# Kernel optimization log

Hardware: AMD Instinct MI355X
Metric: run time of the kernel (lower is better)

## Reference

```python
import jax, jax.numpy as jnp
import numpy as np

RES = 16            # voxel grid resolution (init arg res)
G = RES ** 3        # number of cells = 4096
REG_R = float(np.sqrt(3.0)) / RES  # sqrt(3)/s regularizer radius
B, C, RND, NPTS, H = 16, 64, 2, 16384, 256


def _grid_offsets():
    # util.meshgrid(res): integer grid coords, then ((grid+0.5)/res - 0.5).view(3,-1)
    r = jnp.arange(RES)
    gx, gy, gz = jnp.meshgrid(r, r, r, indexing='ij')
    grid = jnp.stack([gx, gy, gz], 0).reshape(3, -1).astype(jnp.float32)  # [3, G]
    return (grid + 0.5) / RES - 0.5


def _dens_sample(dens, n_points):
    # Deterministic largest-remainder allocation of n_points proportional to density.
    b = dens.shape[0]
    p = dens.reshape(b, -1)
    p = p / jnp.sum(p, axis=-1, keepdims=True)
    scaled = p * n_points                      # [b, G]
    base = jnp.floor(scaled)
    rem = (n_points - jnp.sum(base, axis=-1)).astype(jnp.int32)   # [b]
    frac = scaled - base
    ranks = jnp.argsort(jnp.argsort(-frac, axis=-1), axis=-1)      # rank by fractional part
    return base.astype(jnp.int32) + (ranks < rem[:, None]).astype(jnp.int32)  # [b, G]


def setup_inputs() -> dict:
    key = jax.random.key(0)
    ks = jax.random.split(key, 9)
    cin = C + RND
    f32 = jnp.float32
    return {
        'x': jax.random.normal(ks[0], (B, C, RES, RES, RES), f32),
        'dens': jax.random.uniform(ks[1], (B, RES, RES, RES), f32) + 1e-3,
        'noise': jax.random.uniform(ks[2], (B, RND, NPTS), f32),
        'W1': jax.random.normal(ks[3], (H, cin), f32) * np.float32(1.0 / np.sqrt(cin)),
        'b1': jnp.zeros((H,), f32),
        'W2': jax.random.normal(ks[4], (H, H), f32) * np.float32(1.0 / np.sqrt(H)),
        'b2': jnp.zeros((H,), f32),
        'W3': jax.random.normal(ks[5], (3, H), f32) * np.float32(1.0 / np.sqrt(H)),
        'b3': jnp.zeros((3,), f32),
        'n_points': NPTS,
    }


def reference(x, dens, noise, W1, b1, W2, b2, W3, b3, n_points):
    b, c = x.shape[0], x.shape[1]
    x_flat = x.reshape(b, c, -1)                        # [b, c, G]
    n = _dens_sample(dens, n_points)                    # [b, G] repeat counts, sums to n_points
    # Vectorized replacement for the nonzero()/cat loop: cell i appears n[i] times.
    cell_ids = jnp.arange(G)
    idx = jax.vmap(lambda ni: jnp.repeat(cell_ids, ni, total_repeat_length=n_points))(n)  # [b, n_points]
    x_ind = jnp.take_along_axis(x_flat, idx[:, None, :], axis=2)   # [b, c, n_points]
    o = _grid_offsets()                                 # [3, G]
    gen_off = jnp.transpose(o[:, idx], (1, 0, 2))       # [b, 3, n_points]
    rnd = noise * 2.0 - 1.0                             # uniform in [-1, 1)
    gen_inp = jnp.concatenate([x_ind, rnd], axis=1)     # [b, c+rnd, n_points]
    # pointwise conv1d MLP generator
    h = jax.nn.relu(jnp.einsum('oc,bcn->bon', W1, gen_inp) + b1[:, None])
    h = jax.nn.relu(jnp.einsum('oh,bhn->bon', W2, h) + b2[:, None])
    out = jnp.einsum('oh,bhn->bon', W3, h) + b3[:, None]            # [b, 3, n_points]
    norm = jnp.sqrt(jnp.sum(out * out, axis=1))                      # [b, n_points]
    reg = jnp.maximum(norm - REG_R, 0.0)
    return (out + gen_off, reg)
```

## Files before the change

### kernel.cpp

```cpp
#include <hip/hip_runtime.h>

typedef unsigned long long u64;
typedef _Float16 f16x8 __attribute__((ext_vector_type(8)));
typedef float    f32x4 __attribute__((ext_vector_type(4)));

#define G_    4096
#define NPTS  16384

union H8 { _Float16 h[8]; uint4 u; };
union H4 { _Float16 h[4]; uint2 u; };


__global__ __launch_bounds__(256) void kP(const float* __restrict__ dens,
                                          int* __restrict__ pc,
                                          const float* __restrict__ W1,
                                          const float* __restrict__ W2,
                                          const float* __restrict__ W3,
                                          _Float16* __restrict__ w1f,
                                          _Float16* __restrict__ w2f,
                                          _Float16* __restrict__ w3f,
                                          float* __restrict__ w1n){
  __shared__ double sred[256];
  __shared__ u64  keys[4096];
  __shared__ int  nvs[4096];
  __shared__ int  binidx[4096];
  __shared__ int  hist[1024];
  __shared__ int  cab[1024];
  __shared__ int  scan[256];
  __shared__ float Sf;
  __shared__ int  remS, BstarS, needS, cntS;
  const int t = threadIdx.x;

  if (blockIdx.x >= 16){
    const int e = (blockIdx.x - 16)*256 + t;
    H8 v;
    if (e < 8192){
      const int RT = e >> 9, kt = (e >> 6) & 7, l = e & 63;
      const int m = RT*16 + (l & 15), k = kt*32 + ((l >> 4) << 3);
      #pragma unroll
      for (int j = 0; j < 8; ++j) v.h[j] = (_Float16)W2[m*256 + k + j];
      *(uint4*)&w2f[e*8] = v.u;
    } else if (e < 10240){
      const int e2 = e - 8192;
      const int RT = e2 >> 7, r2 = e2 & 127, kt = r2 >> 6, l = r2 & 63;
      const int m = RT*16 + (l & 15), k = kt*32 + ((l >> 4) << 3);
      #pragma unroll
      for (int j = 0; j < 8; ++j) v.h[j] = (_Float16)W1[m*66 + k + j];
      *(uint4*)&w1f[e2*8] = v.u;
    } else if (e < 10752){
      const int e3 = e - 10240;
      const int kt = e3 >> 6, l = e3 & 63;
      const int m = l & 15, k = kt*32 + ((l >> 4) << 3);
      #pragma unroll
      for (int j = 0; j < 8; ++j) v.h[j] = (m < 3) ? (_Float16)W3[m*256 + k + j] : (_Float16)0.f;
      *(uint4*)&w3f[e3*8] = v.u;
    } else if (e < 11008){
      const int r = e - 10752;
      w1n[r*2 + 0] = W1[r*66 + 64];
      w1n[r*2 + 1] = W1[r*66 + 65];
    }
    return;
  }

  const int b = blockIdx.x;
  const float* d = dens + b*G_;

  for (int j = t; j < 1024; j += 256) hist[j] = 0;
  if (t == 0) cntS = 0;

  double s = 0.0;
  for (int j = 0; j < 16; ++j) s += (double)d[t + 256*j];
  sred[t] = s; __syncthreads();
  for (int off = 128; off > 0; off >>= 1){
    if (t < off) sred[t] += sred[t + off];
    __syncthreads();
  }
  if (t == 0) Sf = (float)sred[0];
  __syncthreads();
  const float S = Sf;

  int bi[16]; int bs = 0;
  #pragma unroll
  for (int j = 0; j < 16; ++j){
    const int i = t + 256*j;
    const float p  = d[i] / S;
    const float sc = p * 16384.0f;
    const float fl = floorf(sc);
    const float fr = sc - fl;
    bi[j] = (int)fl; bs += bi[j];
    const unsigned fb = __float_as_uint(fr);
    keys[i] = ((u64)fb << 12) | (u64)(4095 - i);
    atomicAdd(&hist[fb >> 20], 1);
  }
  scan[t] = bs; __syncthreads();
  for (int off = 128; off > 0; off >>= 1){
    if (t < off) scan[t] += scan[t + off];
    __syncthreads();
  }
  if (t == 0) remS = 16384 - scan[0];
  __syncthreads();
  const int rem = remS;

  const int h0 = hist[4*t], h1 = hist[4*t+1], h2 = hist[4*t+2], h3 = hist[4*t+3];
  const int gs = h0 + h1 + h2 + h3;
  __syncthreads();
  scan[t] = gs; __syncthreads();
  for (int off = 1; off < 256; off <<= 1){
    const int v2 = (t + off < 256) ? scan[t + off] : 0;
    __syncthreads();
    scan[t] += v2;
    __syncthreads();
  }
  const int sAfter = scan[t] - gs;
  cab[4*t+3] = sAfter;
  cab[4*t+2] = sAfter + h3;
  cab[4*t+1] = sAfter + h3 + h2;
  cab[4*t+0] = sAfter + h3 + h2 + h1;
  if (t == 0){ BstarS = 0x7fffffff; needS = 0; }
  __syncthreads();
  if (rem > 0){
    const int ca[4] = {cab[4*t], cab[4*t+1], cab[4*t+2], cab[4*t+3]};
    const int hh[4] = {h0, h1, h2, h3};
    #pragma unroll
    for (int q = 0; q < 4; ++q)
      if (ca[q] < rem && rem <= ca[q] + hh[q]){ BstarS = 4*t + q; needS = rem - ca[q]; }
  }
  __syncthreads();
  const int Bstar = BstarS, need = needS;

  #pragma unroll
  for (int j = 0; j < 16; ++j){
    const int i = t + 256*j;
    const int bin = (int)(keys[i] >> 32);
    nvs[i] = bi[j] + ((bin > Bstar) ? 1 : 0);
    if (bin == Bstar){ const int pos = atomicAdd(&cntS, 1); binidx[pos] = i; }
  }
  __syncthreads();
  const int cnt = cntS;
  for (int p = t; p < cnt; p += 256){
    const u64 K = keys[binidx[p]];
    int r = 0;
    for (int q = 0; q < cnt; ++q) r += (keys[binidx[q]] > K) ? 1 : 0;
    if (r < need) nvs[binidx[p]] += 1;
  }
  __syncthreads();

  int loc[16]; int ls = 0;
  #pragma unroll
  for (int j = 0; j < 16; ++j){ loc[j] = nvs[t*16 + j]; ls += loc[j]; }
  __syncthreads();
  scan[t] = ls; __syncthreads();
  for (int off = 1; off < 256; off <<= 1){
    const int v2 = (t >= off) ? scan[t - off] : 0;
    __syncthreads();
    scan[t] += v2;
    __syncthreads();
  }
  int off0 = scan[t] - ls;
  int* o = pc + b*NPTS;
  #pragma unroll
  for (int j = 0; j < 16; ++j){
    const int c = t*16 + j;
    for (int r = 0; r < loc[j]; ++r) o[off0++] = c;
  }
}

__global__ __launch_bounds__(256, 3) void kE(
    const float* __restrict__ x, const float* __restrict__ noise,
    const _Float16* __restrict__ w1f, const _Float16* __restrict__ w2f,
    const _Float16* __restrict__ w3f, const float* __restrict__ w1n,
    const float* __restrict__ b1, const float* __restrict__ b2, const float* __restrict__ b3,
    const int* __restrict__ pc, float* __restrict__ out)
{
  __shared__ _Float16 Hb[16384];
  __shared__ int   cells[64];
  __shared__ float rndS[2][64];
  const int b = blockIdx.y, p0 = blockIdx.x*64, tid = threadIdx.x;
  const int w = tid >> 6, lane = tid & 63;

  if (tid < 64) cells[tid] = pc[b*NPTS + p0 + tid];
  if (tid >= 64 && tid < 192){
    const int rr = (tid - 64) >> 6, p = tid & 63;
    rndS[rr][p] = noise[(b*2 + rr)*NPTS + p0 + p]*2.f - 1.f;
  }
  __syncthreads();

  {
    const int koct = tid & 3, pt = tid >> 2;
    const int ct = pt >> 4, lane2 = (pt & 15) + koct*16;
    const int cell = cells[pt];
    #pragma unroll
    for (int kt = 0; kt < 2; ++kt){
      const int kbase = kt*32 + koct*8;
      const float* xb = x + ((size_t)(b*64 + kbase))*G_ + cell;
      H8 v;
      #pragma unroll
      for (int j = 0; j < 8; ++j) v.h[j] = (_Float16)xb[(size_t)j*G_];
      *(uint4*)&Hb[((kt*4 + ct)*64 + lane2)*8] = v.u;
    }
  }
  __syncthreads();

  f32x4 acc[4][4];
  const f32x4 zz = {0.f, 0.f, 0.f, 0.f};
  #pragma unroll
  for (int rt = 0; rt < 4; ++rt)
    #pragma unroll
    for (int ct = 0; ct < 4; ++ct) acc[rt][ct] = zz;

  const int wr = w*4;

  __builtin_amdgcn_s_setprio(1);
  #pragma unroll
  for (int kt = 0; kt < 2; ++kt){
    f16x8 B[4];
    #pragma unroll
    for (int ct = 0; ct < 4; ++ct) B[ct] = *(f16x8*)&Hb[((kt*4 + ct)*64 + lane)*8];
    #pragma unroll
    for (int rt = 0; rt < 4; ++rt){
      f16x8 A = *(const f16x8*)&w1f[(((wr + rt)*2 + kt)*64 + lane)*8];
      #pragma unroll
      for (int ct = 0; ct < 4; ++ct)
        acc[rt][ct] = __builtin_amdgcn_mfma_f32_16x16x32_f16(A, B[ct], acc[rt][ct], 0, 0, 0);
    }
  }
  __builtin_amdgcn_s_setprio(0);

  {
    const int m16 = lane & 15, khi = lane >> 4;
    float rn0[4], rn1[4];
    #pragma unroll
    for (int ct = 0; ct < 4; ++ct){
      rn0[ct] = rndS[0][ct*16 + m16];
      rn1[ct] = rndS[1][ct*16 + m16];
    }
    #pragma unroll
    for (int rt = 0; rt < 4; ++rt){
      const int row0 = w*64 + rt*16 + khi*4;
      const float4 wa = *(const float4*)&w1n[row0*2];
      const float4 wb = *(const float4*)&w1n[row0*2 + 4];
      #pragma unroll
      for (int ct = 0; ct < 4; ++ct){
        acc[rt][ct][0] += wa.x*rn0[ct] + wa.y*rn1[ct];
        acc[rt][ct][1] += wa.z*rn0[ct] + wa.w*rn1[ct];
        acc[rt][ct][2] += wb.x*rn0[ct] + wb.y*rn1[ct];
        acc[rt][ct][3] += wb.z*rn0[ct] + wb.w*rn1[ct];
      }
    }
  }
  __syncthreads();

  #pragma unroll
  for (int rt = 0; rt < 4; ++rt){
    const int row0 = w*64 + rt*16 + ((lane >> 4) << 2);
    const float4 bq = *(const float4*)&b1[row0];
    const int kt2 = row0 >> 5, c16 = (row0 >> 3) & 3, j0 = row0 & 7;
    const int lane2 = (lane & 15) + c16*16;
    #pragma unroll
    for (int ct = 0; ct < 4; ++ct){
      H4 v;
      v.h[0] = (_Float16)fmaxf(acc[rt][ct][0] + bq.x, 0.f);
      v.h[1] = (_Float16)fmaxf(acc[rt][ct][1] + bq.y, 0.f);
      v.h[2] = (_Float16)fmaxf(acc[rt][ct][2] + bq.z, 0.f);
      v.h[3] = (_Float16)fmaxf(acc[rt][ct][3] + bq.w, 0.f);
      *(uint2*)&Hb[((kt2*4 + ct)*64 + lane2)*8 + j0] = v.u;
      acc[rt][ct] = zz;
    }
  }
  __syncthreads();

  __builtin_amdgcn_s_setprio(1);
  #pragma unroll 4
  for (int kt = 0; kt < 8; ++kt){
    f16x8 B[4];
    #pragma unroll
    for (int ct = 0; ct < 4; ++ct) B[ct] = *(f16x8*)&Hb[((kt*4 + ct)*64 + lane)*8];
    #pragma unroll
    for (int rt = 0; rt < 4; ++rt){
      f16x8 A = *(const f16x8*)&w2f[(((wr + rt)*8 + kt)*64 + lane)*8];
      #pragma unroll
      for (int ct = 0; ct < 4; ++ct)
        acc[rt][ct] = __builtin_amdgcn_mfma_f32_16x16x32_f16(A, B[ct], acc[rt][ct], 0, 0, 0);
    }
  }
  __builtin_amdgcn_s_setprio(0);
  __syncthreads();

  #pragma unroll
  for (int rt = 0; rt < 4; ++rt){
    const int row0 = w*64 + rt*16 + ((lane >> 4) << 2);
    const float4 bq = *(const float4*)&b2[row0];
    const int kt2 = row0 >> 5, c16 = (row0 >> 3) & 3, j0 = row0 & 7;
    const int lane2 = (lane & 15) + c16*16;
    #pragma unroll
    for (int ct = 0; ct < 4; ++ct){
      H4 v;
      v.h[0] = (_Float16)fmaxf(acc[rt][ct][0] + bq.x, 0.f);
      v.h[1] = (_Float16)fmaxf(acc[rt][ct][1] + bq.y, 0.f);
      v.h[2] = (_Float16)fmaxf(acc[rt][ct][2] + bq.z, 0.f);
      v.h[3] = (_Float16)fmaxf(acc[rt][ct][3] + bq.w, 0.f);
      *(uint2*)&Hb[((kt2*4 + ct)*64 + lane2)*8 + j0] = v.u;
    }
  }
  __syncthreads();

  f32x4 a3 = zz;
  __builtin_amdgcn_s_setprio(1);
  #pragma unroll
  for (int kt = 0; kt < 8; ++kt){
    f16x8 B = *(f16x8*)&Hb[((kt*4 + w)*64 + lane)*8];
    f16x8 A = *(const f16x8*)&w3f[(kt*64 + lane)*8];
    a3 = __builtin_amdgcn_mfma_f32_16x16x32_f16(A, B, a3, 0, 0, 0);
  }
  __builtin_amdgcn_s_setprio(0);
  if (lane < 16){
    const float ox = a3[0] + b3[0];
    const float oy = a3[1] + b3[1];
    const float oz = a3[2] + b3[2];
    const float nrm = sqrtf(ox*ox + oy*oy + oz*oz);
    const float rg_ = fmaxf(nrm - (float)0.10825317547305482, 0.f);
    const int pt = w*16 + lane;
    const int cell = cells[pt];
    const float fx = ((float)(cell >> 8)        + 0.5f) * 0.0625f - 0.5f;
    const float fy = ((float)((cell >> 4) & 15) + 0.5f) * 0.0625f - 0.5f;
    const float fz = ((float)(cell & 15)        + 0.5f) * 0.0625f - 0.5f;
    const int pidx = p0 + pt;
    out[b*49152 +          pidx] = ox + fx;
    out[b*49152 + 16384 +  pidx] = oy + fy;
    out[b*49152 + 32768 +  pidx] = oz + fz;
    out[786432  + b*16384 + pidx] = rg_;
  }
}

extern "C" void kernel_launch(void* const* d_in, const int* in_sizes, int n_in,
                              void* d_out, int out_size, void* d_ws, size_t ws_size,
                              hipStream_t stream){
  const float* x     = (const float*)d_in[0];
  const float* dens  = (const float*)d_in[1];
  const float* noise = (const float*)d_in[2];
  const float* W1    = (const float*)d_in[3];
  const float* b1    = (const float*)d_in[4];
  const float* W2    = (const float*)d_in[5];
  const float* b2    = (const float*)d_in[6];
  const float* W3    = (const float*)d_in[7];
  const float* b3    = (const float*)d_in[8];

  char* ws = (char*)d_ws;
  int*      pc   = (int*)(ws + 0);
  _Float16* w1f  = (_Float16*)(ws + 1048576);
  _Float16* w2f  = (_Float16*)(ws + 1081344);
  _Float16* w3f  = (_Float16*)(ws + 1212416);
  float*    w1n  = (float*)(ws + 1220608);
  float*    out  = (float*)d_out;

  kP<<<dim3(59),      dim3(256), 0, stream>>>(dens, pc, W1, W2, W3, w1f, w2f, w3f, w1n);
  kE<<<dim3(256, 16), dim3(256), 0, stream>>>(x, noise, w1f, w2f, w3f, w1n,
                                              b1, b2, b3, pc, out);
}
```

Baseline: 86.26 us.

## Software-pipeline W2 fragment loads, prefetch W3, drop sync and use packed f16 converts

The layer-2 MFMA loop is fully unrolled with double-buffered A-fragment registers, so the W2 loads for step k+2 are issued between MFMAs of step k. The first two W2 fragments are loaded early, before the noise/bias epilogue of layer 1, and all W3 fragments are loaded into registers before the layer-2 epilogue. The first __syncthreads is removed: each thread reads its cell index straight from global memory rather than through shared memory. Scalar f16 casts become packed round-toward-zero converts, which changes rounding slightly and raises register pressure under the 3-block occupancy bound.

```diff
diff --git a/kernel.cpp b/kernel.cpp
--- a/kernel.cpp
+++ b/kernel.cpp
@@ -3,12 +3,16 @@
 typedef unsigned long long u64;
 typedef _Float16 f16x8 __attribute__((ext_vector_type(8)));
 typedef float    f32x4 __attribute__((ext_vector_type(4)));
+typedef __fp16   fp16x2 __attribute__((ext_vector_type(2)));
 
 #define G_    4096
 #define NPTS  16384
 
 union H8 { _Float16 h[8]; uint4 u; };
-union H4 { _Float16 h[4]; uint2 u; };
+union PK2 { fp16x2 h[2]; uint2 u; };
+union PK4 { fp16x2 h[4]; uint4 u; };
+
+#define MFMA_(A_,B_,C_) __builtin_amdgcn_mfma_f32_16x16x32_f16((A_),(B_),(C_),0,0,0)
 
 
 __global__ __launch_bounds__(256) void kP(const float* __restrict__ dens,
@@ -178,24 +182,28 @@
   const int b = blockIdx.y, p0 = blockIdx.x*64, tid = threadIdx.x;
   const int w = tid >> 6, lane = tid & 63;
 
+  const int pt_g  = tid >> 2;
+  const int cell_g = pc[b*NPTS + p0 + pt_g];
   if (tid < 64) cells[tid] = pc[b*NPTS + p0 + tid];
   if (tid >= 64 && tid < 192){
     const int rr = (tid - 64) >> 6, p = tid & 63;
     rndS[rr][p] = noise[(b*2 + rr)*NPTS + p0 + p]*2.f - 1.f;
   }
-  __syncthreads();
-
   {
-    const int koct = tid & 3, pt = tid >> 2;
-    const int ct = pt >> 4, lane2 = (pt & 15) + koct*16;
-    const int cell = cells[pt];
+    const int koct = tid & 3;
+    const int ct = pt_g >> 4, lane2 = (pt_g & 15) + koct*16;
     #pragma unroll
     for (int kt = 0; kt < 2; ++kt){
       const int kbase = kt*32 + koct*8;
-      const float* xb = x + ((size_t)(b*64 + kbase))*G_ + cell;
-      H8 v;
-      #pragma unroll
-      for (int j = 0; j < 8; ++j) v.h[j] = (_Float16)xb[(size_t)j*G_];
+      const float* xb = x + ((size_t)(b*64 + kbase))*G_ + cell_g;
+      float xv[8];
+      #pragma unroll
+      for (int j = 0; j < 8; ++j) xv[j] = xb[(size_t)j*G_];
+      PK4 v;
+      v.h[0] = __builtin_amdgcn_cvt_pkrtz(xv[0], xv[1]);
+      v.h[1] = __builtin_amdgcn_cvt_pkrtz(xv[2], xv[3]);
+      v.h[2] = __builtin_amdgcn_cvt_pkrtz(xv[4], xv[5]);
+      v.h[3] = __builtin_amdgcn_cvt_pkrtz(xv[6], xv[7]);
       *(uint4*)&Hb[((kt*4 + ct)*64 + lane2)*8] = v.u;
     }
   }
@@ -221,10 +229,17 @@
       f16x8 A = *(const f16x8*)&w1f[(((wr + rt)*2 + kt)*64 + lane)*8];
       #pragma unroll
       for (int ct = 0; ct < 4; ++ct)
-        acc[rt][ct] = __builtin_amdgcn_mfma_f32_16x16x32_f16(A, B[ct], acc[rt][ct], 0, 0, 0);
+        acc[rt][ct] = MFMA_(A, B[ct], acc[rt][ct]);
     }
   }
   __builtin_amdgcn_s_setprio(0);
+
+  f16x8 A0[4], A1[4];
+  #pragma unroll
+  for (int rt = 0; rt < 4; ++rt){
+    A0[rt] = *(const f16x8*)&w2f[(((wr + rt)*8 + 0)*64 + lane)*8];
+    A1[rt] = *(const f16x8*)&w2f[(((wr + rt)*8 + 1)*64 + lane)*8];
+  }
 
   {
     const int m16 = lane & 15, khi = lane >> 4;
@@ -258,11 +273,11 @@
     const int lane2 = (lane & 15) + c16*16;
     #pragma unroll
     for (int ct = 0; ct < 4; ++ct){
-      H4 v;
-      v.h[0] = (_Float16)fmaxf(acc[rt][ct][0] + bq.x, 0.f);
-      v.h[1] = (_Float16)fmaxf(acc[rt][ct][1] + bq.y, 0.f);
-      v.h[2] = (_Float16)fmaxf(acc[rt][ct][2] + bq.z, 0.f);
-      v.h[3] = (_Float16)fmaxf(acc[rt][ct][3] + bq.w, 0.f);
+      PK2 v;
+      v.h[0] = __builtin_amdgcn_cvt_pkrtz(fmaxf(acc[rt][ct][0] + bq.x, 0.f),
+                                          fmaxf(acc[rt][ct][1] + bq.y, 0.f));
+      v.h[1] = __builtin_amdgcn_cvt_pkrtz(fmaxf(acc[rt][ct][2] + bq.z, 0.f),
+                                          fmaxf(acc[rt][ct][3] + bq.w, 0.f));
       *(uint2*)&Hb[((kt2*4 + ct)*64 + lane2)*8 + j0] = v.u;
       acc[rt][ct] = zz;
     }
@@ -270,20 +285,40 @@
   __syncthreads();
 
   __builtin_amdgcn_s_setprio(1);
-  #pragma unroll 4
-  for (int kt = 0; kt < 8; ++kt){
-    f16x8 B[4];
-    #pragma unroll
-    for (int ct = 0; ct < 4; ++ct) B[ct] = *(f16x8*)&Hb[((kt*4 + ct)*64 + lane)*8];
-    #pragma unroll
-    for (int rt = 0; rt < 4; ++rt){
-      f16x8 A = *(const f16x8*)&w2f[(((wr + rt)*8 + kt)*64 + lane)*8];
-      #pragma unroll
-      for (int ct = 0; ct < 4; ++ct)
-        acc[rt][ct] = __builtin_amdgcn_mfma_f32_16x16x32_f16(A, B[ct], acc[rt][ct], 0, 0, 0);
-    }
-  }
+#define MFMA4(AR, RT) \
+    acc[RT][0] = MFMA_(AR, Bv0, acc[RT][0]); \
+    acc[RT][1] = MFMA_(AR, Bv1, acc[RT][1]); \
+    acc[RT][2] = MFMA_(AR, Bv2, acc[RT][2]); \
+    acc[RT][3] = MFMA_(AR, Bv3, acc[RT][3]);
+#define L2STEP(KT, ACUR) { \
+    f16x8 Bv0 = *(f16x8*)&Hb[(((KT)*4 + 0)*64 + lane)*8]; \
+    f16x8 Bv1 = *(f16x8*)&Hb[(((KT)*4 + 1)*64 + lane)*8]; \
+    f16x8 Bv2 = *(f16x8*)&Hb[(((KT)*4 + 2)*64 + lane)*8]; \
+    f16x8 Bv3 = *(f16x8*)&Hb[(((KT)*4 + 3)*64 + lane)*8]; \
+    MFMA4(ACUR[0], 0); \
+    if ((KT) + 2 < 8) ACUR[0] = *(const f16x8*)&w2f[(((wr + 0)*8 + (KT) + 2)*64 + lane)*8]; \
+    MFMA4(ACUR[1], 1); \
+    if ((KT) + 2 < 8) ACUR[1] = *(const f16x8*)&w2f[(((wr + 1)*8 + (KT) + 2)*64 + lane)*8]; \
+    MFMA4(ACUR[2], 2); \
+    if ((KT) + 2 < 8) ACUR[2] = *(const f16x8*)&w2f[(((wr + 2)*8 + (KT) + 2)*64 + lane)*8]; \
+    MFMA4(ACUR[3], 3); \
+    if ((KT) + 2 < 8) ACUR[3] = *(const f16x8*)&w2f[(((wr + 3)*8 + (KT) + 2)*64 + lane)*8]; \
+  }
+  L2STEP(0, A0)
+  L2STEP(1, A1)
+  L2STEP(2, A0)
+  L2STEP(3, A1)
+  L2STEP(4, A0)
+  L2STEP(5, A1)
+  L2STEP(6, A0)
+  L2STEP(7, A1)
+#undef L2STEP
+#undef MFMA4
   __builtin_amdgcn_s_setprio(0);
+
+  f16x8 W3v[8];
+  #pragma unroll
+  for (int kt = 0; kt < 8; ++kt) W3v[kt] = *(const f16x8*)&w3f[(kt*64 + lane)*8];
   __syncthreads();
 
   #pragma unroll
@@ -294,11 +329,11 @@
     const int lane2 = (lane & 15) + c16*16;
     #pragma unroll
     for (int ct = 0; ct < 4; ++ct){
-      H4 v;
-      v.h[0] = (_Float16)fmaxf(acc[rt][ct][0] + bq.x, 0.f);
-      v.h[1] = (_Float16)fmaxf(acc[rt][ct][1] + bq.y, 0.f);
-      v.h[2] = (_Float16)fmaxf(acc[rt][ct][2] + bq.z, 0.f);
-      v.h[3] = (_Float16)fmaxf(acc[rt][ct][3] + bq.w, 0.f);
+      PK2 v;
+      v.h[0] = __builtin_amdgcn_cvt_pkrtz(fmaxf(acc[rt][ct][0] + bq.x, 0.f),
+                                          fmaxf(acc[rt][ct][1] + bq.y, 0.f));
+      v.h[1] = __builtin_amdgcn_cvt_pkrtz(fmaxf(acc[rt][ct][2] + bq.z, 0.f),
+                                          fmaxf(acc[rt][ct][3] + bq.w, 0.f));
       *(uint2*)&Hb[((kt2*4 + ct)*64 + lane2)*8 + j0] = v.u;
     }
   }
@@ -309,8 +344,7 @@
   #pragma unroll
   for (int kt = 0; kt < 8; ++kt){
     f16x8 B = *(f16x8*)&Hb[((kt*4 + w)*64 + lane)*8];
-    f16x8 A = *(const f16x8*)&w3f[(kt*64 + lane)*8];
-    a3 = __builtin_amdgcn_mfma_f32_16x16x32_f16(A, B, a3, 0, 0, 0);
+    a3 = MFMA_(W3v[kt], B, a3);
   }
   __builtin_amdgcn_s_setprio(0);
   if (lane < 16){
```

Result: slower. 90.47 us (+4.9%).

## Pre-transpose x to cell-major fp16 and fold noise into padded W1 MFMA

Applied to the files above, without the earlier changes.

Adds extra prep blocks that transpose x into a per-cell contiguous fp16 layout, so the main kernel gathers 16-byte vectors per point instead of 8 strided fp32 loads. The two noise channels are packed into a third zero-padded K tile of W1, which replaces the scalar fp32 noise FMAs with one more MFMA step. It also preloads the W3 fragments into registers before the last barrier and uses packed round-toward-zero fp16 conversions. The cost is an extra 8 MB workspace write and read in the prep kernel, plus a third MFMA K step that is mostly zeros.

```diff
diff --git a/kernel.cpp b/kernel.cpp
--- a/kernel.cpp
+++ b/kernel.cpp
@@ -3,23 +3,34 @@
 typedef unsigned long long u64;
 typedef _Float16 f16x8 __attribute__((ext_vector_type(8)));
 typedef float    f32x4 __attribute__((ext_vector_type(4)));
+typedef __fp16   fp16x2 __attribute__((ext_vector_type(2)));
 
 #define G_    4096
 #define NPTS  16384
 
 union H8 { _Float16 h[8]; uint4 u; };
-union H4 { _Float16 h[4]; uint2 u; };
-
+union PK2 { fp16x2 h[2]; uint2 u; };
+union PK4 { fp16x2 h[4]; uint4 u; };
+
+#define MFMA_(A_,B_,C_) __builtin_amdgcn_mfma_f32_16x16x32_f16((A_),(B_),(C_),0,0,0)
+
+
+#define OFF_W1F 1048576
+#define OFF_W2F 1097728
+#define OFF_W3F 1228800
+#define OFF_XT  1236992
+#define WS_NEED (OFF_XT + 8388608)
 
 __global__ __launch_bounds__(256) void kP(const float* __restrict__ dens,
                                           int* __restrict__ pc,
                                           const float* __restrict__ W1,
                                           const float* __restrict__ W2,
                                           const float* __restrict__ W3,
+                                          const float* __restrict__ x,
                                           _Float16* __restrict__ w1f,
                                           _Float16* __restrict__ w2f,
                                           _Float16* __restrict__ w3f,
-                                          float* __restrict__ w1n){
+                                          _Float16* __restrict__ xT){
   __shared__ double sred[256];
   __shared__ u64  keys[4096];
   __shared__ int  nvs[4096];
@@ -31,6 +42,27 @@
   __shared__ int  remS, BstarS, needS, cntS;
   const int t = threadIdx.x;
 
+  if (blockIdx.x >= 62){
+    const int idx = blockIdx.x - 62;
+    const int b = idx >> 4, blk = idx & 15;
+    const int cell = blk*256 + t;
+    const float* xb = x + ((size_t)b*64)*G_ + cell;
+    _Float16* xo = xT + ((size_t)(b*G_ + cell))*64;
+    #pragma unroll
+    for (int c8 = 0; c8 < 8; ++c8){
+      float a[8];
+      #pragma unroll
+      for (int j = 0; j < 8; ++j) a[j] = xb[(size_t)(c8*8 + j)*G_];
+      PK4 v;
+      v.h[0] = __builtin_amdgcn_cvt_pkrtz(a[0], a[1]);
+      v.h[1] = __builtin_amdgcn_cvt_pkrtz(a[2], a[3]);
+      v.h[2] = __builtin_amdgcn_cvt_pkrtz(a[4], a[5]);
+      v.h[3] = __builtin_amdgcn_cvt_pkrtz(a[6], a[7]);
+      *(uint4*)&xo[c8*8] = v.u;
+    }
+    return;
+  }
+
   if (blockIdx.x >= 16){
     const int e = (blockIdx.x - 16)*256 + t;
     H8 v;
@@ -40,24 +72,20 @@
       #pragma unroll
       for (int j = 0; j < 8; ++j) v.h[j] = (_Float16)W2[m*256 + k + j];
       *(uint4*)&w2f[e*8] = v.u;
-    } else if (e < 10240){
+    } else if (e < 11264){
       const int e2 = e - 8192;
-      const int RT = e2 >> 7, r2 = e2 & 127, kt = r2 >> 6, l = r2 & 63;
+      const int RT = e2 / 192, r2 = e2 % 192, kt = r2 >> 6, l = r2 & 63;
       const int m = RT*16 + (l & 15), k = kt*32 + ((l >> 4) << 3);
       #pragma unroll
-      for (int j = 0; j < 8; ++j) v.h[j] = (_Float16)W1[m*66 + k + j];
+      for (int j = 0; j < 8; ++j) v.h[j] = (k + j < 66) ? (_Float16)W1[m*66 + k + j] : (_Float16)0.f;
       *(uint4*)&w1f[e2*8] = v.u;
-    } else if (e < 10752){
-      const int e3 = e - 10240;
+    } else if (e < 11776){
+      const int e3 = e - 11264;
       const int kt = e3 >> 6, l = e3 & 63;
       const int m = l & 15, k = kt*32 + ((l >> 4) << 3);
       #pragma unroll
       for (int j = 0; j < 8; ++j) v.h[j] = (m < 3) ? (_Float16)W3[m*256 + k + j] : (_Float16)0.f;
       *(uint4*)&w3f[e3*8] = v.u;
-    } else if (e < 11008){
-      const int r = e - 10752;
-      w1n[r*2 + 0] = W1[r*66 + 64];
-      w1n[r*2 + 1] = W1[r*66 + 65];
     }
     return;
   }
@@ -165,37 +193,54 @@
   }
 }
 
+template<bool USE_XT>
 __global__ __launch_bounds__(256, 3) void kE(
-    const float* __restrict__ x, const float* __restrict__ noise,
+    const float* __restrict__ x, const _Float16* __restrict__ xT,
+    const float* __restrict__ noise,
     const _Float16* __restrict__ w1f, const _Float16* __restrict__ w2f,
-    const _Float16* __restrict__ w3f, const float* __restrict__ w1n,
+    const _Float16* __restrict__ w3f,
     const float* __restrict__ b1, const float* __restrict__ b2, const float* __restrict__ b3,
     const int* __restrict__ pc, float* __restrict__ out)
 {
   __shared__ _Float16 Hb[16384];
-  __shared__ int   cells[64];
-  __shared__ float rndS[2][64];
+  __shared__ int cells[64];
   const int b = blockIdx.y, p0 = blockIdx.x*64, tid = threadIdx.x;
   const int w = tid >> 6, lane = tid & 63;
 
   if (tid < 64) cells[tid] = pc[b*NPTS + p0 + tid];
-  if (tid >= 64 && tid < 192){
-    const int rr = (tid - 64) >> 6, p = tid & 63;
-    rndS[rr][p] = noise[(b*2 + rr)*NPTS + p0 + p]*2.f - 1.f;
-  }
-  __syncthreads();
 
   {
-    const int koct = tid & 3, pt = tid >> 2;
-    const int ct = pt >> 4, lane2 = (pt & 15) + koct*16;
-    const int cell = cells[pt];
-    #pragma unroll
-    for (int kt = 0; kt < 2; ++kt){
-      const int kbase = kt*32 + koct*8;
-      const float* xb = x + ((size_t)(b*64 + kbase))*G_ + cell;
-      H8 v;
-      #pragma unroll
-      for (int j = 0; j < 8; ++j) v.h[j] = (_Float16)xb[(size_t)j*G_];
+    const int ct = tid >> 6, l2 = tid & 63;
+    const int k2 = l2 >> 4, pt = ct*16 + (l2 & 15);
+    PK4 v; v.u = make_uint4(0u, 0u, 0u, 0u);
+    if (k2 == 0){
+      const float n0 = noise[(b*2 + 0)*NPTS + p0 + pt]*2.f - 1.f;
+      const float n1 = noise[(b*2 + 1)*NPTS + p0 + pt]*2.f - 1.f;
+      v.h[0] = __builtin_amdgcn_cvt_pkrtz(n0, n1);
+    }
+    *(uint4*)&Hb[((2*4 + ct)*64 + l2)*8] = v.u;
+  }
+
+  #pragma unroll
+  for (int i = 0; i < 2; ++i){
+    const int e = tid + 256*i;
+    const int pt = e >> 3, koct = e & 7;
+    const int cell = pc[b*NPTS + p0 + pt];
+    const int kt = koct >> 2, k2 = koct & 3;
+    const int lane2 = (pt & 15) + k2*16, ct = pt >> 4;
+    if (USE_XT){
+      const uint4 v = *(const uint4*)&xT[((size_t)(b*G_ + cell))*64 + koct*8];
+      *(uint4*)&Hb[((kt*4 + ct)*64 + lane2)*8] = v;
+    } else {
+      const float* xb = x + ((size_t)(b*64 + koct*8))*G_ + cell;
+      float a[8];
+      #pragma unroll
+      for (int j = 0; j < 8; ++j) a[j] = xb[(size_t)j*G_];
+      PK4 v;
+      v.h[0] = __builtin_amdgcn_cvt_pkrtz(a[0], a[1]);
+      v.h[1] = __builtin_amdgcn_cvt_pkrtz(a[2], a[3]);
+      v.h[2] = __builtin_amdgcn_cvt_pkrtz(a[4], a[5]);
+      v.h[3] = __builtin_amdgcn_cvt_pkrtz(a[6], a[7]);
       *(uint4*)&Hb[((kt*4 + ct)*64 + lane2)*8] = v.u;
     }
   }
@@ -212,42 +257,19 @@
 
   __builtin_amdgcn_s_setprio(1);
   #pragma unroll
-  for (int kt = 0; kt < 2; ++kt){
+  for (int kt = 0; kt < 3; ++kt){
     f16x8 B[4];
     #pragma unroll
     for (int ct = 0; ct < 4; ++ct) B[ct] = *(f16x8*)&Hb[((kt*4 + ct)*64 + lane)*8];
     #pragma unroll
     for (int rt = 0; rt < 4; ++rt){
-      f16x8 A = *(const f16x8*)&w1f[(((wr + rt)*2 + kt)*64 + lane)*8];
+      f16x8 A = *(const f16x8*)&w1f[(((wr + rt)*3 + kt)*64 + lane)*8];
       #pragma unroll
       for (int ct = 0; ct < 4; ++ct)
-        acc[rt][ct] = __builtin_amdgcn_mfma_f32_16x16x32_f16(A, B[ct], acc[rt][ct], 0, 0, 0);
+        acc[rt][ct] = MFMA_(A, B[ct], acc[rt][ct]);
     }
   }
   __builtin_amdgcn_s_setprio(0);
-
-  {
-    const int m16 = lane & 15, khi = lane >> 4;
-    float rn0[4], rn1[4];
-    #pragma unroll
-    for (int ct = 0; ct < 4; ++ct){
-      rn0[ct] = rndS[0][ct*16 + m16];
-      rn1[ct] = rndS[1][ct*16 + m16];
-    }
-    #pragma unroll
-    for (int rt = 0; rt < 4; ++rt){
-      const int row0 = w*64 + rt*16 + khi*4;
-      const float4 wa = *(const float4*)&w1n[row0*2];
-      const float4 wb = *(const float4*)&w1n[row0*2 + 4];
-      #pragma unroll
-      for (int ct = 0; ct < 4; ++ct){
-        acc[rt][ct][0] += wa.x*rn0[ct] + wa.y*rn1[ct];
-        acc[rt][ct][1] += wa.z*rn0[ct] + wa.w*rn1[ct];
-        acc[rt][ct][2] += wb.x*rn0[ct] + wb.y*rn1[ct];
-        acc[rt][ct][3] += wb.z*rn0[ct] + wb.w*rn1[ct];
-      }
-    }
-  }
   __syncthreads();
 
   #pragma unroll
@@ -258,11 +280,11 @@
     const int lane2 = (lane & 15) + c16*16;
     #pragma unroll
     for (int ct = 0; ct < 4; ++ct){
-      H4 v;
-      v.h[0] = (_Float16)fmaxf(acc[rt][ct][0] + bq.x, 0.f);
-      v.h[1] = (_Float16)fmaxf(acc[rt][ct][1] + bq.y, 0.f);
-      v.h[2] = (_Float16)fmaxf(acc[rt][ct][2] + bq.z, 0.f);
-      v.h[3] = (_Float16)fmaxf(acc[rt][ct][3] + bq.w, 0.f);
+      PK2 v;
+      v.h[0] = __builtin_amdgcn_cvt_pkrtz(fmaxf(acc[rt][ct][0] + bq.x, 0.f),
+                                          fmaxf(acc[rt][ct][1] + bq.y, 0.f));
+      v.h[1] = __builtin_amdgcn_cvt_pkrtz(fmaxf(acc[rt][ct][2] + bq.z, 0.f),
+                                          fmaxf(acc[rt][ct][3] + bq.w, 0.f));
       *(uint2*)&Hb[((kt2*4 + ct)*64 + lane2)*8 + j0] = v.u;
       acc[rt][ct] = zz;
     }
@@ -280,10 +302,14 @@
       f16x8 A = *(const f16x8*)&w2f[(((wr + rt)*8 + kt)*64 + lane)*8];
       #pragma unroll
       for (int ct = 0; ct < 4; ++ct)
-        acc[rt][ct] = __builtin_amdgcn_mfma_f32_16x16x32_f16(A, B[ct], acc[rt][ct], 0, 0, 0);
+        acc[rt][ct] = MFMA_(A, B[ct], acc[rt][ct]);
     }
   }
   __builtin_amdgcn_s_setprio(0);
+
+  f16x8 W3v[8];
+  #pragma unroll
+  for (int kt = 0; kt < 8; ++kt) W3v[kt] = *(const f16x8*)&w3f[(kt*64 + lane)*8];
   __syncthreads();
 
   #pragma unroll
@@ -294,11 +320,11 @@
     const int lane2 = (lane & 15) + c16*16;
     #pragma unroll
     for (int ct = 0; ct < 4; ++ct){
-      H4 v;
-      v.h[0] = (_Float16)fmaxf(acc[rt][ct][0] + bq.x, 0.f);
-      v.h[1] = (_Float16)fmaxf(acc[rt][ct][1] + bq.y, 0.f);
-      v.h[2] = (_Float16)fmaxf(acc[rt][ct][2] + bq.z, 0.f);
-      v.h[3] = (_Float16)fmaxf(acc[rt][ct][3] + bq.w, 0.f);
+      PK2 v;
+      v.h[0] = __builtin_amdgcn_cvt_pkrtz(fmaxf(acc[rt][ct][0] + bq.x, 0.f),
+                                          fmaxf(acc[rt][ct][1] + bq.y, 0.f));
+      v.h[1] = __builtin_amdgcn_cvt_pkrtz(fmaxf(acc[rt][ct][2] + bq.z, 0.f),
+                                          fmaxf(acc[rt][ct][3] + bq.w, 0.f));
       *(uint2*)&Hb[((kt2*4 + ct)*64 + lane2)*8 + j0] = v.u;
     }
   }
@@ -309,8 +335,7 @@
   #pragma unroll
   for (int kt = 0; kt < 8; ++kt){
     f16x8 B = *(f16x8*)&Hb[((kt*4 + w)*64 + lane)*8];
-    f16x8 A = *(const f16x8*)&w3f[(kt*64 + lane)*8];
-    a3 = __builtin_amdgcn_mfma_f32_16x16x32_f16(A, B, a3, 0, 0, 0);
+    a3 = MFMA_(W3v[kt], B, a3);
   }
   __builtin_amdgcn_s_setprio(0);
   if (lane < 16){
@@ -347,13 +372,21 @@
 
   char* ws = (char*)d_ws;
   int*      pc   = (int*)(ws + 0);
-  _Float16* w1f  = (_Float16*)(ws + 1048576);
-  _Float16* w2f  = (_Float16*)(ws + 1081344);
-  _Float16* w3f  = (_Float16*)(ws + 1212416);
-  float*    w1n  = (float*)(ws + 1220608);
+  _Float16* w1f  = (_Float16*)(ws + OFF_W1F);
+  _Float16* w2f  = (_Float16*)(ws + OFF_W2F);
+  _Float16* w3f  = (_Float16*)(ws + OFF_W3F);
+  _Float16* xT   = (_Float16*)(ws + OFF_XT);
   float*    out  = (float*)d_out;
 
-  kP<<<dim3(59),      dim3(256), 0, stream>>>(dens, pc, W1, W2, W3, w1f, w2f, w3f, w1n);
-  kE<<<dim3(256, 16), dim3(256), 0, stream>>>(x, noise, w1f, w2f, w3f, w1n,
-                                              b1, b2, b3, pc, out);
+  const bool use_xt = (ws_size >= (size_t)WS_NEED);
+  const int  nprep  = use_xt ? 318 : 62;
+
+  kP<<<dim3(nprep), dim3(256), 0, stream>>>(dens, pc, W1, W2, W3, x,
+                                            w1f, w2f, w3f, xT);
+  if (use_xt)
+    kE<true ><<<dim3(256, 16), dim3(256), 0, stream>>>(x, xT, noise, w1f, w2f, w3f,
+                                                       b1, b2, b3, pc, out);
+  else
+    kE<false><<<dim3(256, 16), dim3(256), 0, stream>>>(x, xT, noise, w1f, w2f, w3f,
+                                                       b1, b2, b3, pc, out);
 }
```

Measured after the change: 84.17 us. 2.4% less time.
